# Kernel optimization log

Hardware: AMD Instinct MI355X
Metric: run time of the kernel (lower is better)

Reference implementation:

```python
import jax, jax.numpy as jnp
import numpy as np
from jax import lax

B, D, F, H = 1024, 64, 8, 256   # batch, state_dim, forcing_dim, hidden_dim
T, TU = 50, 128                  # eval points, forcing samples
N_SUB = 4                        # fixed dopri5 substeps per eval interval


def setup_inputs() -> dict:
    key = jax.random.key(0)
    k1, k2, k3, k4 = jax.random.split(key, 4)
    x0 = jax.random.normal(k1, (B, D), jnp.float32)
    t_eval = jnp.linspace(0.0, 1.0, T, dtype=jnp.float32)
    t_u = jnp.linspace(0.0, 1.0, TU, dtype=jnp.float32)
    u_batch = jax.random.normal(k2, (B, TU, F), jnp.float32)
    W1 = jax.random.normal(k3, (D + F, H), jnp.float32) / np.sqrt(D + F)
    b1 = jnp.zeros((H,), jnp.float32)
    W2 = jax.random.normal(k4, (H, D), jnp.float32) / np.sqrt(H)
    b2 = jnp.zeros((D,), jnp.float32)
    return {"x0": x0, "t_eval": t_eval, "t_u": t_u, "u_batch": u_batch,
            "W1": W1, "b1": b1, "W2": W2, "b2": b2}


def _interp_u(t, t_u, u_batch):
    # piecewise-linear forcing interpolation at scalar time t -> (B, F)
    idx = jnp.clip(jnp.searchsorted(t_u, t, side='right') - 1, 0, t_u.shape[0] - 2)
    t0, t1 = t_u[idx], t_u[idx + 1]
    w = (t - t0) / (t1 - t0)
    u0 = u_batch[:, idx, :]
    u1 = u_batch[:, idx + 1, :]
    return u0 + w * (u1 - u0)


def _odeint_dopri5(f, x0, t_eval):
    # Dormand-Prince RK45 (5th-order solution) with fixed substeps per interval.
    dt_coarse = jnp.diff(t_eval)                                   # [T-1]
    frac = jnp.arange(N_SUB, dtype=x0.dtype) / N_SUB               # [N_SUB]
    ts = (t_eval[:-1, None] + dt_coarse[:, None] * frac).reshape(-1)
    dts = jnp.repeat(dt_coarse / N_SUB, N_SUB)                     # [(T-1)*N_SUB]

    def step(x, tdt):
        t, dt = tdt
        k1 = f(t, x)
        k2 = f(t + dt / 5, x + dt * (k1 / 5))
        k3 = f(t + 3 * dt / 10, x + dt * (3 / 40 * k1 + 9 / 40 * k2))
        k4 = f(t + 4 * dt / 5, x + dt * (44 / 45 * k1 - 56 / 15 * k2 + 32 / 9 * k3))
        k5 = f(t + 8 * dt / 9, x + dt * (19372 / 6561 * k1 - 25360 / 2187 * k2
                                         + 64448 / 6561 * k3 - 212 / 729 * k4))
        k6 = f(t + dt, x + dt * (9017 / 3168 * k1 - 355 / 33 * k2 + 46732 / 5247 * k3
                                 + 49 / 176 * k4 - 5103 / 18656 * k5))
        x_new = x + dt * (35 / 384 * k1 + 500 / 1113 * k3 + 125 / 192 * k4
                          - 2187 / 6784 * k5 + 11 / 84 * k6)
        return x_new, x_new

    _, xs = lax.scan(step, x0, (ts, dts))          # [(T-1)*N_SUB, B, D]
    xs_eval = xs[N_SUB - 1::N_SUB]                  # states at t_eval[1:]
    return jnp.concatenate([x0[None], xs_eval], axis=0)  # [T, B, D]


def reference(x0, t_eval, t_u, u_batch, W1, b1, W2, b2):
    def ode_func(t, x):
        u = _interp_u(t, t_u, u_batch)              # (B, F)
        z = jnp.concatenate([x, u], axis=-1)        # (B, D+F)
        return jnp.tanh(z @ W1 + b1) @ W2 + b2      # (B, D)

    x_tb = _odeint_dopri5(ode_func, x0, t_eval)     # [T, B, D]
    return jnp.transpose(x_tb, (1, 0, 2))           # [B, T, D]
```

## Files before the change

### kernel.cpp

```cpp
#include <hip/hip_runtime.h>


typedef _Float16 half8 __attribute__((ext_vector_type(8)));
typedef float f32x4 __attribute__((ext_vector_type(4)));

#define MFMA16(a, b, c) __builtin_amdgcn_mfma_f32_16x16x32_f16((a), (b), (c), 0, 0, 0)

__global__ __launch_bounds__(256, 2)
void node_kernel(const float* __restrict__ x0,
                 const float* __restrict__ t_eval,
                 const float* __restrict__ t_u,
                 const float* __restrict__ u_batch,
                 const float* __restrict__ W1,
                 const float* __restrict__ b1,
                 const float* __restrict__ W2,
                 const float* __restrict__ b2,
                 float* __restrict__ out)
{
    __shared__ __align__(16) _Float16 zAh[12 * 144];
    __shared__ __align__(16) _Float16 hAh[32 * 144];
    __shared__ __align__(16) float ush[6][2][8];

    const int tid = threadIdx.x;
    const int wv  = tid >> 6;
    const int l   = tid & 63;
    const int lm  = l & 15;
    const int lq  = l >> 4;
    const int blk = blockIdx.x;

    const float C2L = 2.8853900817779268f;

    for (int i = tid; i < (12 * 144) / 2; i += 256) ((uint32_t*)zAh)[i] = 0u;
    for (int i = tid; i < (32 * 144) / 2; i += 256) ((uint32_t*)hAh)[i] = 0u;

    half8 b1h[4][3], b1l[4][3];
    float b1b[4];
#pragma unroll
    for (int t = 0; t < 4; ++t) {
        const int n1 = (wv * 4 + t) * 16 + lm;
        b1b[t] = b1[n1] * C2L;
#pragma unroll
        for (int c = 0; c < 3; ++c) {
#pragma unroll
            for (int j = 0; j < 8; ++j) {
                const int k = c * 32 + lq * 8 + j;
                const float v = (k < 72) ? W1[k * 256 + n1] * C2L : 0.0f;
                const _Float16 hi = (_Float16)v;
                b1h[t][c][j] = hi;
                b1l[t][c][j] = (_Float16)(v - (float)hi);
            }
        }
    }

    const int n2 = wv * 16 + lm;
    half8 b2h[8];
#pragma unroll
    for (int cc = 0; cc < 8; ++cc) {
#pragma unroll
        for (int j = 0; j < 8; ++j) {
            const int k = cc * 32 + lq * 8 + j;
            b2h[cc][j] = (_Float16)W2[k * 64 + n2];
        }
    }
    const float b2b = b2[n2];

    float xr[2];
    float kfr[5][2];
#pragma unroll
    for (int r = 0; r < 2; ++r) {
        const int gr = blk * 2 + r;
        xr[r] = x0[gr * 64 + n2];
        if (lq == 0) out[gr * 3200 + n2] = xr[r];
    }
    __syncthreads();

#pragma unroll 1
    for (int step = 0; step < 196; ++step) {
        const int n = step >> 2;
        const int m = step & 3;
        const float te0 = t_eval[n];
        const float dtc = t_eval[n + 1] - te0;
        const float t   = te0 + dtc * (0.25f * (float)m);
        const float dt  = dtc * 0.25f;

        if (tid < 96) {
            const int s   = tid >> 4;
            const int rem = tid & 15;
            const int mr  = rem >> 3, f = rem & 7;
            float cs;
            switch (s) {
                case 0: cs = 0.0f; break;
                case 1: cs = 1.0f / 5.0f; break;
                case 2: cs = 3.0f / 10.0f; break;
                case 3: cs = 4.0f / 5.0f; break;
                case 4: cs = 8.0f / 9.0f; break;
                default: cs = 1.0f; break;
            }
            const float tsv = t + dt * cs;
            int iu = (int)(tsv * 127.0f);
            iu = iu < 0 ? 0 : (iu > 126 ? 126 : iu);
            const float ta = t_u[iu];
            const float tb = t_u[iu + 1];
            const float wt = (tsv - ta) / (tb - ta);
            const float* ub = &u_batch[(blk * 2 + mr) * 1024 + iu * 8 + f];
            const float u0v = ub[0];
            const float u1v = ub[8];
            ush[s][mr][f] = fmaf(wt, u1v - u0v, u0v);
        }
        __syncthreads();

#pragma unroll
        for (int s = 0; s < 6; ++s) {
            float zv[2];
#pragma unroll
            for (int r = 0; r < 2; ++r) {
                float v;
                if (s == 0)      v = xr[r];
                else if (s == 1) v = fmaf(dt, kfr[0][r] * (1.0f/5.0f), xr[r]);
                else if (s == 2) v = fmaf(dt, fmaf(3.0f/40.0f, kfr[0][r], (9.0f/40.0f)*kfr[1][r]), xr[r]);
                else if (s == 3) v = fmaf(dt, (44.0f/45.0f)*kfr[0][r] + (-56.0f/15.0f)*kfr[1][r]
                                             + (32.0f/9.0f)*kfr[2][r], xr[r]);
                else if (s == 4) v = fmaf(dt, (19372.0f/6561.0f)*kfr[0][r] + (-25360.0f/2187.0f)*kfr[1][r]
                                             + (64448.0f/6561.0f)*kfr[2][r] + (-212.0f/729.0f)*kfr[3][r], xr[r]);
                else             v = fmaf(dt, (9017.0f/3168.0f)*kfr[0][r] + (-355.0f/33.0f)*kfr[1][r]
                                             + (46732.0f/5247.0f)*kfr[2][r] + (49.0f/176.0f)*kfr[3][r]
                                             + (-5103.0f/18656.0f)*kfr[4][r], xr[r]);
                zv[r] = v;
            }
            if (lq == 0) {
#pragma unroll
                for (int r = 0; r < 2; ++r)
                    zAh[(n2 >> 3) * 144 + r * 8 + (n2 & 7)] = (_Float16)zv[r];
            }
            if (wv == 1 && l < 8) {
                const int mm = l >> 2;
                const int jj = (l & 3) * 2;
                const _Float16 u0h = (_Float16)ush[s][mm][jj];
                const _Float16 u1h = (_Float16)ush[s][mm][jj + 1];
                uint32_t pk = (uint32_t)*(const uint16_t*)&u0h
                            | ((uint32_t)*(const uint16_t*)&u1h << 16);
                *(uint32_t*)&zAh[8 * 144 + mm * 8 + jj] = pk;
            }
            __syncthreads();

            half8 az[3];
#pragma unroll
            for (int c = 0; c < 3; ++c)
                az[c] = *(const half8*)&zAh[(c * 4 + lq) * 144 + lm * 8];
#pragma unroll
            for (int t = 0; t < 4; ++t) {
                f32x4 aHH = {0.f, 0.f, 0.f, 0.f};
                f32x4 aHL = {0.f, 0.f, 0.f, 0.f};
#pragma unroll
                for (int c = 0; c < 3; ++c) {
                    aHH = MFMA16(az[c], b1h[t][c], aHH);
                    aHL = MFMA16(az[c], b1l[t][c], aHL);
                }
                const int kqb = (wv * 4 + t) * 2 + (lm >> 3);
#pragma unroll
                for (int r = 0; r < 2; ++r) {
                    const float y = aHH[r] + aHL[r] + b1b[t];
                    const float e = __builtin_amdgcn_exp2f(y);
                    const float hv = fmaf(-2.0f, __builtin_amdgcn_rcpf(e + 1.0f), 1.0f);
                    if (lq == 0)
                        hAh[kqb * 144 + r * 8 + (lm & 7)] = (_Float16)hv;
                }
            }
            __syncthreads();

            f32x4 aP = {0.f, 0.f, 0.f, 0.f};
            f32x4 aR = {0.f, 0.f, 0.f, 0.f};
#pragma unroll
            for (int cc = 0; cc < 8; cc += 2) {
                const half8 ah0 = *(const half8*)&hAh[((cc    ) * 4 + lq) * 144 + lm * 8];
                const half8 ah1 = *(const half8*)&hAh[((cc + 1) * 4 + lq) * 144 + lm * 8];
                aP = MFMA16(ah0, b2h[cc    ], aP);
                aR = MFMA16(ah1, b2h[cc + 1], aR);
            }
            if (s < 5) {
#pragma unroll
                for (int r = 0; r < 2; ++r)
                    kfr[s][r] = (aP[r] + aR[r]) + b2b;
            } else {
#pragma unroll
                for (int r = 0; r < 2; ++r) {
                    const float k6 = (aP[r] + aR[r]) + b2b;
                    xr[r] = fmaf(dt, (35.0f/384.0f)*kfr[0][r] + (500.0f/1113.0f)*kfr[2][r]
                                    + (125.0f/192.0f)*kfr[3][r] + (-2187.0f/6784.0f)*kfr[4][r]
                                    + (11.0f/84.0f)*k6, xr[r]);
                }
            }
        }

        if (m == 3 && lq == 0) {
#pragma unroll
            for (int r = 0; r < 2; ++r)
                out[(blk * 2 + r) * 3200 + (n + 1) * 64 + n2] = xr[r];
        }
    }
}

extern "C" void kernel_launch(void* const* d_in, const int* in_sizes, int n_in,
                              void* d_out, int out_size, void* d_ws, size_t ws_size,
                              hipStream_t stream) {
    const float* x0      = (const float*)d_in[0];
    const float* t_eval  = (const float*)d_in[1];
    const float* t_u     = (const float*)d_in[2];
    const float* u_batch = (const float*)d_in[3];
    const float* W1      = (const float*)d_in[4];
    const float* b1      = (const float*)d_in[5];
    const float* W2      = (const float*)d_in[6];
    const float* b2      = (const float*)d_in[7];
    float* out = (float*)d_out;

    node_kernel<<<dim3(512), dim3(256), 0, stream>>>(
        x0, t_eval, t_u, u_batch, W1, b1, W2, b2, out);
}
```

Baseline: 1.201 ms.

## Process one batch row per block and drop split-precision W1 MFMAs

Each block now handles a single batch row instead of two, doubling the grid to 1024 blocks and raising the launch-bounds occupancy target to 4 blocks per SM. The hi/lo fp16 split of W1 is removed, halving the first-layer MFMA count and the registers that held the low parts. Because a row is serialized through 196 steps, more blocks give more parallel latency hiding. The cost is lower W1 precision and more redundant weight loading per block.

```diff
diff --git a/kernel.cpp b/kernel.cpp
--- a/kernel.cpp
+++ b/kernel.cpp
@@ -6,7 +6,7 @@
 
 #define MFMA16(a, b, c) __builtin_amdgcn_mfma_f32_16x16x32_f16((a), (b), (c), 0, 0, 0)
 
-__global__ __launch_bounds__(256, 2)
+__global__ __launch_bounds__(256, 4)
 void node_kernel(const float* __restrict__ x0,
                  const float* __restrict__ t_eval,
                  const float* __restrict__ t_u,
@@ -19,7 +19,7 @@
 {
     __shared__ __align__(16) _Float16 zAh[12 * 144];
     __shared__ __align__(16) _Float16 hAh[32 * 144];
-    __shared__ __align__(16) float ush[6][2][8];
+    __shared__ __align__(16) float ush[6][8];
 
     const int tid = threadIdx.x;
     const int wv  = tid >> 6;
@@ -33,7 +33,7 @@
     for (int i = tid; i < (12 * 144) / 2; i += 256) ((uint32_t*)zAh)[i] = 0u;
     for (int i = tid; i < (32 * 144) / 2; i += 256) ((uint32_t*)hAh)[i] = 0u;
 
-    half8 b1h[4][3], b1l[4][3];
+    half8 b1h[4][3];
     float b1b[4];
 #pragma unroll
     for (int t = 0; t < 4; ++t) {
@@ -44,10 +44,7 @@
 #pragma unroll
             for (int j = 0; j < 8; ++j) {
                 const int k = c * 32 + lq * 8 + j;
-                const float v = (k < 72) ? W1[k * 256 + n1] * C2L : 0.0f;
-                const _Float16 hi = (_Float16)v;
-                b1h[t][c][j] = hi;
-                b1l[t][c][j] = (_Float16)(v - (float)hi);
+                b1h[t][c][j] = (_Float16)((k < 72) ? W1[k * 256 + n1] * C2L : 0.0f);
             }
         }
     }
@@ -64,14 +61,9 @@
     }
     const float b2b = b2[n2];
 
-    float xr[2];
-    float kfr[5][2];
-#pragma unroll
-    for (int r = 0; r < 2; ++r) {
-        const int gr = blk * 2 + r;
-        xr[r] = x0[gr * 64 + n2];
-        if (lq == 0) out[gr * 3200 + n2] = xr[r];
-    }
+    float xr = x0[blk * 64 + n2];
+    float kfr[5];
+    if (lq == 0) out[blk * 3200 + n2] = xr;
     __syncthreads();
 
 #pragma unroll 1
@@ -83,10 +75,9 @@
         const float t   = te0 + dtc * (0.25f * (float)m);
         const float dt  = dtc * 0.25f;
 
-        if (tid < 96) {
-            const int s   = tid >> 4;
-            const int rem = tid & 15;
-            const int mr  = rem >> 3, f = rem & 7;
+        if (tid < 48) {
+            const int s = tid >> 3;
+            const int f = tid & 7;
             float cs;
             switch (s) {
                 case 0: cs = 0.0f; break;
@@ -102,44 +93,35 @@
             const float ta = t_u[iu];
             const float tb = t_u[iu + 1];
             const float wt = (tsv - ta) / (tb - ta);
-            const float* ub = &u_batch[(blk * 2 + mr) * 1024 + iu * 8 + f];
+            const float* ub = &u_batch[blk * 1024 + iu * 8 + f];
             const float u0v = ub[0];
             const float u1v = ub[8];
-            ush[s][mr][f] = fmaf(wt, u1v - u0v, u0v);
+            ush[s][f] = fmaf(wt, u1v - u0v, u0v);
         }
         __syncthreads();
 
 #pragma unroll
         for (int s = 0; s < 6; ++s) {
-            float zv[2];
-#pragma unroll
-            for (int r = 0; r < 2; ++r) {
-                float v;
-                if (s == 0)      v = xr[r];
-                else if (s == 1) v = fmaf(dt, kfr[0][r] * (1.0f/5.0f), xr[r]);
-                else if (s == 2) v = fmaf(dt, fmaf(3.0f/40.0f, kfr[0][r], (9.0f/40.0f)*kfr[1][r]), xr[r]);
-                else if (s == 3) v = fmaf(dt, (44.0f/45.0f)*kfr[0][r] + (-56.0f/15.0f)*kfr[1][r]
-                                             + (32.0f/9.0f)*kfr[2][r], xr[r]);
-                else if (s == 4) v = fmaf(dt, (19372.0f/6561.0f)*kfr[0][r] + (-25360.0f/2187.0f)*kfr[1][r]
-                                             + (64448.0f/6561.0f)*kfr[2][r] + (-212.0f/729.0f)*kfr[3][r], xr[r]);
-                else             v = fmaf(dt, (9017.0f/3168.0f)*kfr[0][r] + (-355.0f/33.0f)*kfr[1][r]
-                                             + (46732.0f/5247.0f)*kfr[2][r] + (49.0f/176.0f)*kfr[3][r]
-                                             + (-5103.0f/18656.0f)*kfr[4][r], xr[r]);
-                zv[r] = v;
-            }
-            if (lq == 0) {
-#pragma unroll
-                for (int r = 0; r < 2; ++r)
-                    zAh[(n2 >> 3) * 144 + r * 8 + (n2 & 7)] = (_Float16)zv[r];
-            }
-            if (wv == 1 && l < 8) {
-                const int mm = l >> 2;
-                const int jj = (l & 3) * 2;
-                const _Float16 u0h = (_Float16)ush[s][mm][jj];
-                const _Float16 u1h = (_Float16)ush[s][mm][jj + 1];
+            float zv;
+            if (s == 0)      zv = xr;
+            else if (s == 1) zv = fmaf(dt, kfr[0] * (1.0f/5.0f), xr);
+            else if (s == 2) zv = fmaf(dt, fmaf(3.0f/40.0f, kfr[0], (9.0f/40.0f)*kfr[1]), xr);
+            else if (s == 3) zv = fmaf(dt, (44.0f/45.0f)*kfr[0] + (-56.0f/15.0f)*kfr[1]
+                                          + (32.0f/9.0f)*kfr[2], xr);
+            else if (s == 4) zv = fmaf(dt, (19372.0f/6561.0f)*kfr[0] + (-25360.0f/2187.0f)*kfr[1]
+                                          + (64448.0f/6561.0f)*kfr[2] + (-212.0f/729.0f)*kfr[3], xr);
+            else             zv = fmaf(dt, (9017.0f/3168.0f)*kfr[0] + (-355.0f/33.0f)*kfr[1]
+                                          + (46732.0f/5247.0f)*kfr[2] + (49.0f/176.0f)*kfr[3]
+                                          + (-5103.0f/18656.0f)*kfr[4], xr);
+            if (lq == 0)
+                zAh[(n2 >> 3) * 144 + (n2 & 7)] = (_Float16)zv;
+            if (wv == 1 && l < 4) {
+                const int jj = l * 2;
+                const _Float16 u0h = (_Float16)ush[s][jj];
+                const _Float16 u1h = (_Float16)ush[s][jj + 1];
                 uint32_t pk = (uint32_t)*(const uint16_t*)&u0h
                             | ((uint32_t)*(const uint16_t*)&u1h << 16);
-                *(uint32_t*)&zAh[8 * 144 + mm * 8 + jj] = pk;
+                *(uint32_t*)&zAh[8 * 144 + jj] = pk;
             }
             __syncthreads();
 
@@ -150,21 +132,15 @@
 #pragma unroll
             for (int t = 0; t < 4; ++t) {
                 f32x4 aHH = {0.f, 0.f, 0.f, 0.f};
-                f32x4 aHL = {0.f, 0.f, 0.f, 0.f};
 #pragma unroll
-                for (int c = 0; c < 3; ++c) {
+                for (int c = 0; c < 3; ++c)
                     aHH = MFMA16(az[c], b1h[t][c], aHH);
-                    aHL = MFMA16(az[c], b1l[t][c], aHL);
-                }
                 const int kqb = (wv * 4 + t) * 2 + (lm >> 3);
-#pragma unroll
-                for (int r = 0; r < 2; ++r) {
-                    const float y = aHH[r] + aHL[r] + b1b[t];
-                    const float e = __builtin_amdgcn_exp2f(y);
-                    const float hv = fmaf(-2.0f, __builtin_amdgcn_rcpf(e + 1.0f), 1.0f);
-                    if (lq == 0)
-                        hAh[kqb * 144 + r * 8 + (lm & 7)] = (_Float16)hv;
-                }
+                const float y = aHH[0] + b1b[t];
+                const float e = __builtin_amdgcn_exp2f(y);
+                const float hv = fmaf(-2.0f, __builtin_amdgcn_rcpf(e + 1.0f), 1.0f);
+                if (lq == 0)
+                    hAh[kqb * 144 + (lm & 7)] = (_Float16)hv;
             }
             __syncthreads();
 
@@ -178,25 +154,17 @@
                 aR = MFMA16(ah1, b2h[cc + 1], aR);
             }
             if (s < 5) {
-#pragma unroll
-                for (int r = 0; r < 2; ++r)
-                    kfr[s][r] = (aP[r] + aR[r]) + b2b;
+                kfr[s] = (aP[0] + aR[0]) + b2b;
             } else {
-#pragma unroll
-                for (int r = 0; r < 2; ++r) {
-                    const float k6 = (aP[r] + aR[r]) + b2b;
-                    xr[r] = fmaf(dt, (35.0f/384.0f)*kfr[0][r] + (500.0f/1113.0f)*kfr[2][r]
-                                    + (125.0f/192.0f)*kfr[3][r] + (-2187.0f/6784.0f)*kfr[4][r]
-                                    + (11.0f/84.0f)*k6, xr[r]);
-                }
+                const float k6 = (aP[0] + aR[0]) + b2b;
+                xr = fmaf(dt, (35.0f/384.0f)*kfr[0] + (500.0f/1113.0f)*kfr[2]
+                             + (125.0f/192.0f)*kfr[3] + (-2187.0f/6784.0f)*kfr[4]
+                             + (11.0f/84.0f)*k6, xr);
             }
         }
 
-        if (m == 3 && lq == 0) {
-#pragma unroll
-            for (int r = 0; r < 2; ++r)
-                out[(blk * 2 + r) * 3200 + (n + 1) * 64 + n2] = xr[r];
-        }
+        if (m == 3 && lq == 0)
+            out[blk * 3200 + (n + 1) * 64 + n2] = xr;
     }
 }
 
@@ -213,6 +181,6 @@
     const float* b2      = (const float*)d_in[7];
     float* out = (float*)d_out;
 
-    node_kernel<<<dim3(512), dim3(256), 0, stream>>>(
+    node_kernel<<<dim3(1024), dim3(256), 0, stream>>>(
         x0, t_eval, t_u, u_batch, W1, b1, W2, b2, out);
 }
```

Measured after the change: 1.281 ms. 1.07x slower.

## Drop split-precision W1 MFMAs and compute forcing term in fp32 FMAs

Applied to the files above, without the earlier changes.

Removes the low-half fp16 correction MFMAs for W1, so the first layer uses a single fp16 MFMA chain instead of hi+lo pairs. The K dimension shrinks from 96 to 64: the 8 forcing inputs are no longer packed into shared memory as fp16 but applied as an fp32 FMA dot product per hidden unit, then distributed to MFMA lanes with shuffles. This halves the layer-1 MFMA count and cuts one chunk of K padding. In exchange the x·W1 term loses the low-order correction and gains fp16 rounding error, which may affect accuracy over 196 integration steps.

```diff
diff --git a/kernel.cpp b/kernel.cpp
--- a/kernel.cpp
+++ b/kernel.cpp
@@ -17,7 +17,7 @@
                  const float* __restrict__ b2,
                  float* __restrict__ out)
 {
-    __shared__ __align__(16) _Float16 zAh[12 * 144];
+    __shared__ __align__(16) _Float16 zAh[8 * 144];
     __shared__ __align__(16) _Float16 hAh[32 * 144];
     __shared__ __align__(16) float ush[6][2][8];
 
@@ -30,27 +30,29 @@
 
     const float C2L = 2.8853900817779268f;
 
-    for (int i = tid; i < (12 * 144) / 2; i += 256) ((uint32_t*)zAh)[i] = 0u;
+    for (int i = tid; i < (8 * 144) / 2; i += 256)  ((uint32_t*)zAh)[i] = 0u;
     for (int i = tid; i < (32 * 144) / 2; i += 256) ((uint32_t*)hAh)[i] = 0u;
 
-    half8 b1h[4][3], b1l[4][3];
+    half8 b1h[4][2];
     float b1b[4];
 #pragma unroll
     for (int t = 0; t < 4; ++t) {
         const int n1 = (wv * 4 + t) * 16 + lm;
         b1b[t] = b1[n1] * C2L;
 #pragma unroll
-        for (int c = 0; c < 3; ++c) {
+        for (int c = 0; c < 2; ++c) {
 #pragma unroll
             for (int j = 0; j < 8; ++j) {
                 const int k = c * 32 + lq * 8 + j;
-                const float v = (k < 72) ? W1[k * 256 + n1] * C2L : 0.0f;
-                const _Float16 hi = (_Float16)v;
-                b1h[t][c][j] = hi;
-                b1l[t][c][j] = (_Float16)(v - (float)hi);
-            }
-        }
-    }
+                b1h[t][c][j] = (_Float16)(W1[k * 256 + n1] * C2L);
+            }
+        }
+    }
+    const int n1u = wv * 64 + l;
+    float w1u[8];
+#pragma unroll
+    for (int f = 0; f < 8; ++f)
+        w1u[f] = W1[(64 + f) * 256 + n1u] * C2L;
 
     const int n2 = wv * 16 + lm;
     half8 b2h[8];
@@ -132,38 +134,50 @@
                 for (int r = 0; r < 2; ++r)
                     zAh[(n2 >> 3) * 144 + r * 8 + (n2 & 7)] = (_Float16)zv[r];
             }
-            if (wv == 1 && l < 8) {
-                const int mm = l >> 2;
-                const int jj = (l & 3) * 2;
-                const _Float16 u0h = (_Float16)ush[s][mm][jj];
-                const _Float16 u1h = (_Float16)ush[s][mm][jj + 1];
-                uint32_t pk = (uint32_t)*(const uint16_t*)&u0h
-                            | ((uint32_t)*(const uint16_t*)&u1h << 16);
-                *(uint32_t*)&zAh[8 * 144 + mm * 8 + jj] = pk;
-            }
             __syncthreads();
 
-            half8 az[3];
-#pragma unroll
-            for (int c = 0; c < 3; ++c)
+            const float4 uA0 = *(const float4*)&ush[s][0][0];
+            const float4 uB0 = *(const float4*)&ush[s][0][4];
+            const float4 uA1 = *(const float4*)&ush[s][1][0];
+            const float4 uB1 = *(const float4*)&ush[s][1][4];
+            float yu0 = uA0.x * w1u[0];
+            yu0 = fmaf(uA0.y, w1u[1], yu0);
+            yu0 = fmaf(uA0.z, w1u[2], yu0);
+            yu0 = fmaf(uA0.w, w1u[3], yu0);
+            yu0 = fmaf(uB0.x, w1u[4], yu0);
+            yu0 = fmaf(uB0.y, w1u[5], yu0);
+            yu0 = fmaf(uB0.z, w1u[6], yu0);
+            yu0 = fmaf(uB0.w, w1u[7], yu0);
+            float yu1 = uA1.x * w1u[0];
+            yu1 = fmaf(uA1.y, w1u[1], yu1);
+            yu1 = fmaf(uA1.z, w1u[2], yu1);
+            yu1 = fmaf(uA1.w, w1u[3], yu1);
+            yu1 = fmaf(uB1.x, w1u[4], yu1);
+            yu1 = fmaf(uB1.y, w1u[5], yu1);
+            yu1 = fmaf(uB1.z, w1u[6], yu1);
+            yu1 = fmaf(uB1.w, w1u[7], yu1);
+
+            half8 az[2];
+#pragma unroll
+            for (int c = 0; c < 2; ++c)
                 az[c] = *(const half8*)&zAh[(c * 4 + lq) * 144 + lm * 8];
 #pragma unroll
             for (int t = 0; t < 4; ++t) {
                 f32x4 aHH = {0.f, 0.f, 0.f, 0.f};
-                f32x4 aHL = {0.f, 0.f, 0.f, 0.f};
-#pragma unroll
-                for (int c = 0; c < 3; ++c) {
-                    aHH = MFMA16(az[c], b1h[t][c], aHH);
-                    aHL = MFMA16(az[c], b1l[t][c], aHL);
-                }
+                aHH = MFMA16(az[0], b1h[t][0], aHH);
+                aHH = MFMA16(az[1], b1h[t][1], aHH);
+                const float yut0 = __shfl(yu0, t * 16 + lm);
+                const float yut1 = __shfl(yu1, t * 16 + lm);
                 const int kqb = (wv * 4 + t) * 2 + (lm >> 3);
-#pragma unroll
-                for (int r = 0; r < 2; ++r) {
-                    const float y = aHH[r] + aHL[r] + b1b[t];
-                    const float e = __builtin_amdgcn_exp2f(y);
-                    const float hv = fmaf(-2.0f, __builtin_amdgcn_rcpf(e + 1.0f), 1.0f);
-                    if (lq == 0)
-                        hAh[kqb * 144 + r * 8 + (lm & 7)] = (_Float16)hv;
+                const float y0 = aHH[0] + yut0 + b1b[t];
+                const float y1 = aHH[1] + yut1 + b1b[t];
+                const float e0 = __builtin_amdgcn_exp2f(y0);
+                const float e1 = __builtin_amdgcn_exp2f(y1);
+                const float h0 = fmaf(-2.0f, __builtin_amdgcn_rcpf(e0 + 1.0f), 1.0f);
+                const float h1 = fmaf(-2.0f, __builtin_amdgcn_rcpf(e1 + 1.0f), 1.0f);
+                if (lq == 0) {
+                    hAh[kqb * 144 + (lm & 7)]     = (_Float16)h0;
+                    hAh[kqb * 144 + 8 + (lm & 7)] = (_Float16)h1;
                 }
             }
             __syncthreads();
```

New measurement: 1.160 ms. 3.4% less time.

## Drop fp16 hi/lo split for W1 and compact LDS operand buffers with zero-row aliasing

Applied to the files above, without the earlier changes.

Removes the low-part compensation MFMAs for the first layer so W1 is used in plain fp16, halving layer-1 matrix instructions and freeing registers. Shrinks the z and h LDS staging buffers to hold only the two real batch rows plus one shared zero row, with padding lanes all reading that zero row. This cuts LDS footprint and traffic but lowers first-layer precision, which could affect accuracy over the long integration.

```diff
diff --git a/kernel.cpp b/kernel.cpp
--- a/kernel.cpp
+++ b/kernel.cpp
@@ -17,8 +17,8 @@
                  const float* __restrict__ b2,
                  float* __restrict__ out)
 {
-    __shared__ __align__(16) _Float16 zAh[12 * 144];
-    __shared__ __align__(16) _Float16 hAh[32 * 144];
+    __shared__ __align__(16) _Float16 zAh[12 * 24];
+    __shared__ __align__(16) _Float16 hAh[32 * 24];
     __shared__ __align__(16) float ush[6][2][8];
 
     const int tid = threadIdx.x;
@@ -30,10 +30,14 @@
 
     const float C2L = 2.8853900817779268f;
 
-    for (int i = tid; i < (12 * 144) / 2; i += 256) ((uint32_t*)zAh)[i] = 0u;
-    for (int i = tid; i < (32 * 144) / 2; i += 256) ((uint32_t*)hAh)[i] = 0u;
-
-    half8 b1h[4][3], b1l[4][3];
+    for (int i = tid; i < (12 * 24) / 2; i += 256) ((uint32_t*)zAh)[i] = 0u;
+    for (int i = tid; i < (32 * 24) / 2; i += 256) ((uint32_t*)hAh)[i] = 0u;
+
+    const int rowoff = (lm < 2 ? lm : 2) * 16;
+    const char* zb = (const char*)zAh + lq * 48 + rowoff;
+    const char* hb = (const char*)hAh + lq * 48 + rowoff;
+
+    half8 b1h[4][3];
     float b1b[4];
 #pragma unroll
     for (int t = 0; t < 4; ++t) {
@@ -44,10 +48,7 @@
 #pragma unroll
             for (int j = 0; j < 8; ++j) {
                 const int k = c * 32 + lq * 8 + j;
-                const float v = (k < 72) ? W1[k * 256 + n1] * C2L : 0.0f;
-                const _Float16 hi = (_Float16)v;
-                b1h[t][c][j] = hi;
-                b1l[t][c][j] = (_Float16)(v - (float)hi);
+                b1h[t][c][j] = (_Float16)((k < 72) ? W1[k * 256 + n1] * C2L : 0.0f);
             }
         }
     }
@@ -130,7 +131,7 @@
             if (lq == 0) {
 #pragma unroll
                 for (int r = 0; r < 2; ++r)
-                    zAh[(n2 >> 3) * 144 + r * 8 + (n2 & 7)] = (_Float16)zv[r];
+                    zAh[(n2 >> 3) * 24 + r * 8 + (n2 & 7)] = (_Float16)zv[r];
             }
             if (wv == 1 && l < 8) {
                 const int mm = l >> 2;
@@ -139,31 +140,29 @@
                 const _Float16 u1h = (_Float16)ush[s][mm][jj + 1];
                 uint32_t pk = (uint32_t)*(const uint16_t*)&u0h
                             | ((uint32_t)*(const uint16_t*)&u1h << 16);
-                *(uint32_t*)&zAh[8 * 144 + mm * 8 + jj] = pk;
+                *(uint32_t*)&zAh[8 * 24 + mm * 8 + jj] = pk;
             }
             __syncthreads();
 
-            half8 az[3];
-#pragma unroll
-            for (int c = 0; c < 3; ++c)
-                az[c] = *(const half8*)&zAh[(c * 4 + lq) * 144 + lm * 8];
+            const half8 az0 = *(const half8*)(zb);
+            const half8 az1 = *(const half8*)(zb + 192);
+            const half8 az2 = *(const half8*)(zb + 384);
 #pragma unroll
             for (int t = 0; t < 4; ++t) {
                 f32x4 aHH = {0.f, 0.f, 0.f, 0.f};
-                f32x4 aHL = {0.f, 0.f, 0.f, 0.f};
-#pragma unroll
-                for (int c = 0; c < 3; ++c) {
-                    aHH = MFMA16(az[c], b1h[t][c], aHH);
-                    aHL = MFMA16(az[c], b1l[t][c], aHL);
-                }
-                const int kqb = (wv * 4 + t) * 2 + (lm >> 3);
-#pragma unroll
-                for (int r = 0; r < 2; ++r) {
-                    const float y = aHH[r] + aHL[r] + b1b[t];
-                    const float e = __builtin_amdgcn_exp2f(y);
-                    const float hv = fmaf(-2.0f, __builtin_amdgcn_rcpf(e + 1.0f), 1.0f);
-                    if (lq == 0)
-                        hAh[kqb * 144 + r * 8 + (lm & 7)] = (_Float16)hv;
+                aHH = MFMA16(az0, b1h[t][0], aHH);
+                aHH = MFMA16(az1, b1h[t][1], aHH);
+                aHH = MFMA16(az2, b1h[t][2], aHH);
+                const int pl = (wv * 4 + t) * 2 + (lm >> 3);
+                const float y0 = aHH[0] + b1b[t];
+                const float y1 = aHH[1] + b1b[t];
+                const float e0 = __builtin_amdgcn_exp2f(y0);
+                const float e1 = __builtin_amdgcn_exp2f(y1);
+                const float h0 = fmaf(-2.0f, __builtin_amdgcn_rcpf(e0 + 1.0f), 1.0f);
+                const float h1 = fmaf(-2.0f, __builtin_amdgcn_rcpf(e1 + 1.0f), 1.0f);
+                if (lq == 0) {
+                    hAh[pl * 24 + (lm & 7)]     = (_Float16)h0;
+                    hAh[pl * 24 + 8 + (lm & 7)] = (_Float16)h1;
                 }
             }
             __syncthreads();
@@ -172,8 +171,8 @@
             f32x4 aR = {0.f, 0.f, 0.f, 0.f};
 #pragma unroll
             for (int cc = 0; cc < 8; cc += 2) {
-                const half8 ah0 = *(const half8*)&hAh[((cc    ) * 4 + lq) * 144 + lm * 8];
-                const half8 ah1 = *(const half8*)&hAh[((cc + 1) * 4 + lq) * 144 + lm * 8];
+                const half8 ah0 = *(const half8*)(hb + cc * 192);
+                const half8 ah1 = *(const half8*)(hb + cc * 192 + 192);
                 aP = MFMA16(ah0, b2h[cc    ], aP);
                 aR = MFMA16(ah1, b2h[cc + 1], aR);
             }
```

Result: faster. 1.011 ms (-15.8%).
